# Kernel tuning notes

Measured on AMD Instinct MI355X. Metric: run time of the kernel, lower is better.

Reference implementation:

```python
import jax, jax.numpy as jnp
import numpy as np

B, T, D, H = 2, 2048, 1024, 16
DH = D // H
PD = 6
SCALE = DH ** -0.5
_PAIRS4 = [(0, 1), (0, 2), (0, 3), (1, 2), (1, 3), (2, 3)]
_J6 = jnp.array([[0, 0, 0, 0, 0, 1], [0, 0, 0, 0, -1, 0], [0, 0, 0, 1, 0, 0],
                 [0, 0, 1, 0, 0, 0], [0, -1, 0, 0, 0, 0], [1, 0, 0, 0, 0, 0]], dtype=jnp.float32)


def exterior(p1, p2):
    # p1, p2: (..., 4) -> normalized 6-d Plucker line (..., 6)
    parts = [p1[..., i] * p2[..., j] - p1[..., j] * p2[..., i] for i, j in _PAIRS4]
    L = jnp.stack(parts, axis=-1)
    n = jnp.linalg.norm(L, axis=-1, keepdims=True)
    return L / jnp.clip(n, 1e-12)


def setup_inputs() -> dict:
    key = jax.random.key(0)
    ks = jax.random.split(key, 12)
    s = 0.02
    return {
        'x': jax.random.normal(ks[0], (B, T, D), jnp.float32),
        'qkv_w': jax.random.normal(ks[1], (D, 3 * D), jnp.float32) * s,
        'qkv_b': jnp.zeros((3 * D,), jnp.float32),
        'w1_write': jax.random.normal(ks[2], (D, 4 * H), jnp.float32) * s,
        'w2_write': jax.random.normal(ks[3], (D, 4 * H), jnp.float32) * s,
        'w1_read': jax.random.normal(ks[4], (D, 4 * H), jnp.float32) * s,
        'w2_read': jax.random.normal(ks[5], (D, 4 * H), jnp.float32) * s,
        'memv_w': jax.random.normal(ks[6], (D, D), jnp.float32) * s,
        'memv_b': jnp.zeros((D,), jnp.float32),
        'memg_w': jax.random.normal(ks[7], (D, H), jnp.float32) * s,
        'memg_b': jnp.zeros((H,), jnp.float32),
        'mem_scale': jnp.full((H,), 0.1, jnp.float32),
        'rw_mix': jnp.zeros((), jnp.float32),
        'out_w': jax.random.normal(ks[8], (D, D), jnp.float32) * s,
        'out_b': jnp.zeros((D,), jnp.float32),
        'decay_logits': jnp.full((H,), 4.6, jnp.float32),
    }


def reference(x, qkv_w, qkv_b, w1_write, w2_write, w1_read, w2_read,
              memv_w, memv_b, memg_w, memg_b, mem_scale, rw_mix,
              out_w, out_b, decay_logits):
    # ---- standard causal softmax attention ----
    qkv = (x @ qkv_w + qkv_b).reshape(B, T, 3, H, DH).transpose(2, 0, 3, 1, 4)
    q, k, v = qkv[0], qkv[1], qkv[2]                      # each (B,H,T,DH)
    scores = jnp.einsum('bhtd,bhsd->bhts', q, k) * SCALE
    mask = jnp.triu(jnp.ones((T, T), bool), 1)
    scores = jnp.where(mask[None, None], -jnp.inf, scores)
    attn = jax.nn.softmax(scores, axis=-1)                # dropout=0 (eval)
    seq_out = jnp.einsum('bhts,bhsd->bthd', attn, v).reshape(B, T, D)

    # ---- Plucker lines for write (prev->cur) and read ----
    x_prev = jnp.concatenate([jnp.zeros((B, 1, D), x.dtype), x[:, :-1]], axis=1)
    w1 = (x_prev @ w1_write).reshape(B, T, H, 4)
    w2 = (x @ w2_write).reshape(B, T, H, 4)
    write_lines = exterior(w1, w2)                        # (B,T,H,6)
    r1 = (x @ w1_read).reshape(B, T, H, 4)
    r2 = (x @ w2_read).reshape(B, T, H, 4)
    read_lines = exterior(r1, r2)

    Jw = jnp.einsum('bthi,ij->bhtj', write_lines, _J6)    # (B,H,T,6)
    Jr = jnp.einsum('bthi,ij->bhtj', read_lines, _J6)
    rd = read_lines.transpose(0, 2, 1, 3)                 # (B,H,T,6)

    # ---- decay-weighted cumsum of 6x6 outer-product states ----
    decays = jax.nn.sigmoid(decay_logits)                 # (H,)
    pos = jnp.arange(T, dtype=x.dtype)
    decay_inv = (1.0 / jnp.clip(decays, 1e-6))[:, None] ** pos[None]   # (H,T)
    decay_fwd = decays[:, None] ** pos[None]                           # (H,T)

    def shifted_state(Jv):
        outer = Jv[..., :, None] * Jv[..., None, :]       # (B,H,T,6,6)
        ow = outer * decay_inv[None, :, :, None, None]
        M = jnp.cumsum(ow, axis=2)
        M = jnp.concatenate([jnp.zeros((B, H, 1, PD, PD), x.dtype), M[:, :, :-1]], axis=2)
        return M * decay_fwd[None, :, :, None, None]

    Mw = shifted_state(Jw)
    Mr = shifted_state(Jr)

    score_w = jnp.einsum('bhti,bhtij,bhtj->bht', rd, Mw, rd)
    score_r = jnp.einsum('bhti,bhtij,bhtj->bht', Jw, Mr, Jw)
    alpha = jax.nn.sigmoid(rw_mix)
    mem_score = (1 - alpha) * score_w + alpha * score_r   # (B,H,T)

    mem_val = x @ memv_w + memv_b                         # (B,T,D)
    gate = jax.nn.sigmoid(x @ memg_w + memg_b)            # (B,T,H)
    mem_score_t = mem_score.transpose(0, 2, 1)            # (B,T,H)
    gated = jax.nn.sigmoid(mem_score_t * mem_scale[None, None, :]) * gate
    gated = gated.mean(axis=-1, keepdims=True)            # (B,T,1)

    return (seq_out + gated * mem_val) @ out_w + out_b
```

## Files before the change

### kernel.cpp

```cpp
#include <hip/hip_runtime.h>

#define Bb 2
#define Tt 2048
#define Dd 1024
#define Hh 16
#define LDC 4480

typedef __attribute__((ext_vector_type(8))) short s16x8;
typedef __attribute__((ext_vector_type(4))) float f32x4;
typedef __attribute__((ext_vector_type(8))) _Float16 f16x8;

__device__ __forceinline__ float bf2f(unsigned short u) {
  unsigned v = ((unsigned)u) << 16;
  union { unsigned u; float f; } c; c.u = v; return c.f;
}
__device__ __forceinline__ unsigned short f2bf(float f) {
  union { float f; unsigned u; } c; c.f = f;
  unsigned u = c.u + 0x7fffu + ((c.u >> 16) & 1u);
  return (unsigned short)(u >> 16);
}
__device__ __forceinline__ float sigm(float x) { return 1.f / (1.f + expf(-x)); }

typedef const __attribute__((address_space(1))) void* gas_ptr;
typedef __attribute__((address_space(3))) void* las_ptr;
__device__ __forceinline__ void gload_lds16(const unsigned short* g, unsigned short* l) {
  __builtin_amdgcn_global_load_lds((gas_ptr)g, (las_ptr)l, 16, 0, 0);
}



__global__ __launch_bounds__(256) void prep_kernel(const float* __restrict__ x,
                                                   const float* __restrict__ qkv_w,
                                                   const float* __restrict__ w1w,
                                                   const float* __restrict__ w2w,
                                                   const float* __restrict__ w1r,
                                                   const float* __restrict__ w2r,
                                                   const float* __restrict__ memg_w,
                                                   const float* __restrict__ memv_w,
                                                   const float* __restrict__ out_w,
                                                   const float* __restrict__ qkv_b,
                                                   const float* __restrict__ memg_b,
                                                   const float* __restrict__ memv_b,
                                                   unsigned short* __restrict__ xb,
                                                   unsigned short* __restrict__ WT,
                                                   unsigned short* __restrict__ outT,
                                                   float* __restrict__ biasC) {
  __shared__ float tile[32][33];
  int id = blockIdx.x;
  if (id < 2048) {
    int i = id * 256 + threadIdx.x;
    int row = i >> 7;
    int k8 = i & 127;
    const float4* xv = reinterpret_cast<const float4*>(x + (size_t)i * 8);
    float4 a = xv[0], b = xv[1];
    s16x8 out;
    out[0] = (short)f2bf(a.x); out[1] = (short)f2bf(a.y);
    out[2] = (short)f2bf(a.z); out[3] = (short)f2bf(a.w);
    out[4] = (short)f2bf(b.x); out[5] = (short)f2bf(b.y);
    out[6] = (short)f2bf(b.z); out[7] = (short)f2bf(b.w);
    int mt = row >> 4, kt = k8 >> 2, quad = k8 & 3;
    int lane = (row & 15) + quad * 16;
    *(s16x8*)&xb[(((size_t)mt * 32 + kt) * 64 + lane) * 8] = out;
  } else if (id < 6528) {
    int j = id - 2048;
    int n0 = (j % 140) * 32, kt = j / 140, k0 = kt * 32;
    int tx = threadIdx.x & 31, ty = threadIdx.x >> 5;
#pragma unroll
    for (int i = 0; i < 4; i++) {
      int k = k0 + ty + i * 8, n = n0 + tx;
      float v;
      if (n < 3072)       v = qkv_w[(size_t)k * 3072 + n];
      else if (n < 3136)  v = w1w[k * 64 + (n - 3072)];
      else if (n < 3200)  v = w2w[k * 64 + (n - 3136)];
      else if (n < 3264)  v = w1r[k * 64 + (n - 3200)];
      else if (n < 3328)  v = w2r[k * 64 + (n - 3264)];
      else if (n < 3344)  v = memg_w[k * 16 + (n - 3328)];
      else if (n < 3392)  v = 0.f;
      else if (n < 4416)  v = memv_w[(size_t)k * 1024 + (n - 3392)];
      else                v = 0.f;
      tile[ty + i * 8][tx] = v;
    }
    __syncthreads();
    if (threadIdx.x < 128) {
      int nl = threadIdx.x & 31, quad = threadIdx.x >> 5;
      s16x8 out;
#pragma unroll
      for (int e = 0; e < 8; e++) out[e] = (short)f2bf(tile[quad * 8 + e][nl]);
      int nt = (n0 >> 4) + (nl >> 4);
      int lane = (nl & 15) + quad * 16;
      *(s16x8*)&WT[(((size_t)nt * 32 + kt) * 64 + lane) * 8] = out;
    }
  } else if (id < 7552) {
    int j = id - 6528;
    int n0 = (j & 31) * 32, kt = j >> 5, k0 = kt * 32;
    int tx = threadIdx.x & 31, ty = threadIdx.x >> 5;
#pragma unroll
    for (int i = 0; i < 4; i++) {
      int k = k0 + ty + i * 8, n = n0 + tx;
      tile[ty + i * 8][tx] = out_w[(size_t)k * 1024 + n];
    }
    __syncthreads();
    if (threadIdx.x < 128) {
      int nl = threadIdx.x & 31, quad = threadIdx.x >> 5;
      s16x8 out;
#pragma unroll
      for (int e = 0; e < 8; e++) out[e] = (short)f2bf(tile[quad * 8 + e][nl]);
      int nt = (n0 >> 4) + (nl >> 4);
      int lane = (nl & 15) + quad * 16;
      *(s16x8*)&outT[(((size_t)nt * 32 + kt) * 64 + lane) * 8] = out;
    }
  } else {
    int i = (id - 7552) * 256 + threadIdx.x;
    if (i < LDC) {
      float v = 0.f;
      if (i < 3072) v = qkv_b[i];
      else if (i >= 3328 && i < 3344) v = memg_b[i - 3328];
      else if (i >= 3392 && i < 4416) v = memv_b[i - 3392];
      biasC[i] = v;
    }
  }
}


template <int MODE>
__global__ __launch_bounds__(256) void gemm_frag_kernel(const unsigned short* __restrict__ Af,
                                                        const unsigned short* __restrict__ Bf,
                                                        void* __restrict__ Cout,
                                                        const float* __restrict__ bias) {
  __shared__ __align__(16) unsigned short lds[2][16][512];
  int mTile, nTile;
  if (MODE == 0) {
    const int xx = blockIdx.x & 7, local = blockIdx.x >> 3;
    mTile = (xx >> 1) * 8 + (local & 7);
    nTile = (xx & 1) * 18 + (local >> 3);
    if (nTile >= 35) return;
  } else {
    mTile = blockIdx.x >> 3;
    nTile = blockIdx.x & 7;
  }
  const int lane = threadIdx.x & 63, wid = threadIdx.x >> 6;
  const int quad = lane >> 4, c16 = lane & 15;
  const int wm = wid >> 1, wn = wid & 1;
  const int mt0 = mTile * 8 + wm * 4;
  const int nt0 = nTile * 8 + wn * 4;

  const unsigned short* src[4];
#pragma unroll
  for (int i = 0; i < 4; i++) {
    int f = wid * 4 + i;
    src[i] = ((f < 8) ? (Af + (size_t)(mTile * 8 + f) * 16384)
                      : (Bf + (size_t)(nTile * 8 + (f - 8)) * 16384))
             + (size_t)lane * 8;
  }

  f32x4 acc[4][4] = {};

#pragma unroll
  for (int i = 0; i < 4; i++) gload_lds16(src[i], &lds[0][wid * 4 + i][0]);
  __syncthreads();

  int buf = 0;
  for (int kt = 0; kt < 32; kt++) {
    if (kt + 1 < 32) {
#pragma unroll
      for (int i = 0; i < 4; i++)
        gload_lds16(src[i] + (size_t)(kt + 1) * 512, &lds[buf ^ 1][wid * 4 + i][0]);
    }
    s16x8 a[4], b[4];
#pragma unroll
    for (int i = 0; i < 4; i++) {
      a[i] = *(const s16x8*)&lds[buf][wm * 4 + i][lane * 8];
      b[i] = *(const s16x8*)&lds[buf][8 + wn * 4 + i][lane * 8];
    }
#pragma unroll
    for (int mt = 0; mt < 4; mt++)
#pragma unroll
      for (int nt = 0; nt < 4; nt++)
        acc[mt][nt] = __builtin_amdgcn_mfma_f32_16x16x32_bf16(a[mt], b[nt],
                                                              acc[mt][nt], 0, 0, 0);
    __syncthreads();
    buf ^= 1;
  }

#pragma unroll
  for (int mt = 0; mt < 4; mt++)
#pragma unroll
    for (int nt = 0; nt < 4; nt++) {
      int col = (nt0 + nt) * 16 + c16;
      float bv = bias[col];
#pragma unroll
      for (int r = 0; r < 4; r++) {
        int row = (mt0 + mt) * 16 + quad * 4 + r;
        if (MODE == 0)
          ((unsigned short*)Cout)[(size_t)row * 4480 + col] = f2bf(acc[mt][nt][r] + bv);
        else
          ((float*)Cout)[(size_t)row * 1024 + col] = acc[mt][nt][r] + bv;
      }
    }
}


__device__ __forceinline__ void ext6(const float* p, const float* q, float* L) {
  L[0] = p[0] * q[1] - p[1] * q[0];
  L[1] = p[0] * q[2] - p[2] * q[0];
  L[2] = p[0] * q[3] - p[3] * q[0];
  L[3] = p[1] * q[2] - p[2] * q[1];
  L[4] = p[1] * q[3] - p[3] * q[1];
  L[5] = p[2] * q[3] - p[3] * q[2];
  float n = sqrtf(L[0]*L[0] + L[1]*L[1] + L[2]*L[2] + L[3]*L[3] + L[4]*L[4] + L[5]*L[5]);
  float inv = 1.f / fmaxf(n, 1e-12f);
#pragma unroll
  for (int k = 0; k < 6; k++) L[k] *= inv;
}


__global__ __launch_bounds__(256) void post1_kernel(const unsigned short* __restrict__ Cq,
                                                    unsigned short* __restrict__ Kt,
                                                    unsigned short* __restrict__ Vt,
                                                    float* __restrict__ Jw,
                                                    float* __restrict__ Jr,
                                                    float* __restrict__ rd) {
  __shared__ unsigned short vt[32 * 66];
  int id = blockIdx.x;
  int tid = threadIdx.x;
  if (id < 2048) {
    int kb = id & 63, bh = id >> 6;
    int b = bh >> 4, h = bh & 15;
    size_t tbase = ((size_t)bh * 64 + kb) * 2048;
    {
      int key = tid >> 3, p = tid & 7, dg = p ^ (key & 7);
      size_t src = (size_t)(b * Tt + kb * 32 + key) * LDC + 1024 + h * 64 + dg * 8;
      s16x8 kv = *(const s16x8*)&Cq[src];
      s16x8 kvs;
#pragma unroll
      for (int e = 0; e < 8; e++)
        kvs[e] = (short)f2bf(bf2f((unsigned short)kv[e]) * 0.125f);
      *(s16x8*)&Kt[tbase + (size_t)tid * 8] = kvs;
    }
    {
      int row = tid >> 3, c = tid & 7;
      size_t src = (size_t)(b * Tt + kb * 32 + row) * LDC + 2048 + h * 64 + c * 8;
      s16x8 vv = *(const s16x8*)&Cq[src];
#pragma unroll
      for (int e = 0; e < 8; e++) {
        union { _Float16 hf; unsigned short s; } cv;
        cv.hf = (_Float16)bf2f((unsigned short)vv[e]);
        vt[row * 66 + c * 8 + e] = cv.s;
      }
    }
    __syncthreads();
    {
      int d = tid >> 2, p = tid & 3, cq = p ^ ((d >> 2) & 3);
      s16x8 out;
#pragma unroll
      for (int e = 0; e < 8; e++) {
        int key = ((e >> 2) & 1) * 16 + cq * 4 + (e & 3);
        out[e] = (short)vt[key * 66 + d];
      }
      *(s16x8*)&Vt[tbase + (size_t)tid * 8] = out;
    }
  } else {
    int idx = (id - 2048) * 256 + tid;
    int h = idx & 15, t = (idx >> 4) & 2047, b = idx >> 15;
    size_t row = (size_t)(b * Tt + t) * LDC;
    float w1[4], w2[4], r1[4], r2[4];
#pragma unroll
    for (int k = 0; k < 4; k++) {
      w1[k] = (t > 0) ? bf2f(Cq[row - LDC + 3072 + h * 4 + k]) : 0.f;
      w2[k] = bf2f(Cq[row + 3136 + h * 4 + k]);
      r1[k] = bf2f(Cq[row + 3200 + h * 4 + k]);
      r2[k] = bf2f(Cq[row + 3264 + h * 4 + k]);
    }
    float Lw[6], Lr[6];
    ext6(w1, w2, Lw);
    ext6(r1, r2, Lr);
    size_t ob = ((size_t)(b * Hh + h) * Tt + t) * 6;
    Jw[ob + 0] = Lw[5]; Jw[ob + 1] = -Lw[4]; Jw[ob + 2] = Lw[3];
    Jw[ob + 3] = Lw[2]; Jw[ob + 4] = -Lw[1]; Jw[ob + 5] = Lw[0];
    Jr[ob + 0] = Lr[5]; Jr[ob + 1] = -Lr[4]; Jr[ob + 2] = Lr[3];
    Jr[ob + 3] = Lr[2]; Jr[ob + 4] = -Lr[1]; Jr[ob + 5] = Lr[0];
#pragma unroll
    for (int k = 0; k < 6; k++) rd[ob + k] = Lr[k];
  }
}


__device__ __forceinline__ void do_tile(int ks, int q0, int quad, int c16,
                                        const s16x8& qf0, const s16x8& qf1,
                                        const s16x8 kf[2][2], const f16x8 vb[4],
                                        float& l_i, f32x4 o[4]) {
  f32x4 st0 = {}, st1 = {};
  __builtin_amdgcn_s_setprio(1);
  st0 = __builtin_amdgcn_mfma_f32_16x16x32_bf16(kf[0][0], qf0, st0, 0, 0, 0);
  st0 = __builtin_amdgcn_mfma_f32_16x16x32_bf16(kf[0][1], qf1, st0, 0, 0, 0);
  st1 = __builtin_amdgcn_mfma_f32_16x16x32_bf16(kf[1][0], qf0, st1, 0, 0, 0);
  st1 = __builtin_amdgcn_mfma_f32_16x16x32_bf16(kf[1][1], qf1, st1, 0, 0, 0);
  __builtin_amdgcn_s_setprio(0);
  bool need_mask = (ks + 31 > q0);
  f16x8 pa;
  float lp = 0.f;
#pragma unroll
  for (int r = 0; r < 4; r++) {
    float v0 = st0[r];
    float v1 = st1[r];
    if (need_mask) {
      v0 = (ks + quad * 4 + r      <= q0 + c16) ? v0 : -1e30f;
      v1 = (ks + 16 + quad * 4 + r <= q0 + c16) ? v1 : -1e30f;
    }
    float p0 = __expf(v0);
    float p1 = __expf(v1);
    lp += p0 + p1;
    pa[r]     = (_Float16)p0;
    pa[4 + r] = (_Float16)p1;
  }
  l_i += lp;
  __builtin_amdgcn_s_setprio(1);
#pragma unroll
  for (int nt = 0; nt < 4; nt++)
    o[nt] = __builtin_amdgcn_mfma_f32_16x16x32_f16(pa, vb[nt], o[nt], 0, 0, 0);
  __builtin_amdgcn_s_setprio(0);
}

__global__ __launch_bounds__(128, 2) void attn_kernel(const unsigned short* __restrict__ Cq,
                                                      const unsigned short* __restrict__ Kt,
                                                      const unsigned short* __restrict__ Vt,
                                                      unsigned short* __restrict__ po) {
  __shared__ float mrg[64][69];
  const int id = blockIdx.x;
  const int xcd = id & 7, rest = id >> 3;
  const int j = rest & 31;
  const int bh = ((rest >> 5) << 3) | xcd;
  const int b = bh >> 4, h = bh & 15;
  const int kw = threadIdx.x >> 6, lane = threadIdx.x & 63;
  const int quad = lane >> 4, c16 = lane & 15;
  const int qA0r = j * 32,        qA1r = j * 32 + 16;
  const int qB0r = 2016 - j * 32, qB1r = 2032 - j * 32;
  const int Ttot = 64 - j;
  const int ht = (j >= 16) ? 16 : (32 - j);
  const int t0 = kw ? ht : 0;
  const int t1 = kw ? Ttot : ht;
  const char* Kbase = (const char*)(Kt + (size_t)bh * 64 * 2048);
  const char* Vbase = (const char*)(Vt + (size_t)bh * 64 * 2048);
  const int vK0 = c16 * 128 + ((quad       ^ (c16 & 7)) * 16);
  const int vK1 = c16 * 128 + (((4 + quad) ^ (c16 & 7)) * 16);
  const int vV  = c16 * 64  + ((quad ^ ((c16 >> 2) & 3)) * 16);

  size_t rowA0 = (size_t)(b * Tt + qA0r + c16) * LDC + h * 64;
  size_t rowA1 = (size_t)(b * Tt + qA1r + c16) * LDC + h * 64;
  size_t rowB0 = (size_t)(b * Tt + qB0r + c16) * LDC + h * 64;
  size_t rowB1 = (size_t)(b * Tt + qB1r + c16) * LDC + h * 64;
  s16x8 qa00 = *(const s16x8*)&Cq[rowA0 + quad * 8];
  s16x8 qa01 = *(const s16x8*)&Cq[rowA0 + 32 + quad * 8];
  s16x8 qa10 = *(const s16x8*)&Cq[rowA1 + quad * 8];
  s16x8 qa11 = *(const s16x8*)&Cq[rowA1 + 32 + quad * 8];
  s16x8 qb00 = *(const s16x8*)&Cq[rowB0 + quad * 8];
  s16x8 qb01 = *(const s16x8*)&Cq[rowB0 + 32 + quad * 8];
  s16x8 qb10 = *(const s16x8*)&Cq[rowB1 + quad * 8];
  s16x8 qb11 = *(const s16x8*)&Cq[rowB1 + 32 + quad * 8];

  float lA0 = 0.f, lA1 = 0.f, lB0 = 0.f, lB1 = 0.f;
  f32x4 oA0[4] = {}, oA1[4] = {}, oB0[4] = {}, oB1[4] = {};

  s16x8 kfX[2][2], kfY[2][2];
  f16x8 vbX[4], vbY[4];

#define LOADT(dstK, dstV, kb) do {                                   \
    const char* Kb_ = Kbase + (size_t)(kb) * 4096;                   \
    const char* Vb_ = Vbase + (size_t)(kb) * 4096;                   \
    dstK[0][0] = *(const s16x8*)(Kb_ + vK0);                         \
    dstK[0][1] = *(const s16x8*)(Kb_ + vK1);                         \
    dstK[1][0] = *(const s16x8*)(Kb_ + 2048 + vK0);                  \
    dstK[1][1] = *(const s16x8*)(Kb_ + 2048 + vK1);                  \
    dstV[0] = *(const f16x8*)(Vb_ + vV);                             \
    dstV[1] = *(const f16x8*)(Vb_ + 1024 + vV);                      \
    dstV[2] = *(const f16x8*)(Vb_ + 2048 + vV);                      \
    dstV[3] = *(const f16x8*)(Vb_ + 3072 + vV);                      \
  } while (0)

#define DOTILES(KF, VF, t) do {                                      \
    int ks_ = (t) * 32;                                              \
    do_tile(ks_, qB0r, quad, c16, qb00, qb01, KF, VF, lB0, oB0);     \
    do_tile(ks_, qB1r, quad, c16, qb10, qb11, KF, VF, lB1, oB1);     \
    if ((t) <= j) {                                                  \
      do_tile(ks_, qA0r, quad, c16, qa00, qa01, KF, VF, lA0, oA0);   \
      do_tile(ks_, qA1r, quad, c16, qa10, qa11, KF, VF, lA1, oA1);   \
    }                                                                \
  } while (0)

  LOADT(kfX, vbX, t0);
  for (int t = t0; t < t1; t += 2) {
    if (t + 1 < t1) LOADT(kfY, vbY, t + 1);
    DOTILES(kfX, vbX, t);
    if (t + 1 < t1) {
      if (t + 2 < t1) LOADT(kfX, vbX, t + 2);
      DOTILES(kfY, vbY, t + 1);
    }
  }
#undef DOTILES
#undef LOADT

  if (kw == 1) {
#pragma unroll
    for (int nt = 0; nt < 4; nt++)
#pragma unroll
      for (int r = 0; r < 4; r++) {
        mrg[lane][nt * 4 + r]      = oB0[nt][r];
        mrg[lane][16 + nt * 4 + r] = oB1[nt][r];
        mrg[lane][32 + nt * 4 + r] = oA0[nt][r];
        mrg[lane][48 + nt * 4 + r] = oA1[nt][r];
      }
    mrg[lane][64] = lB0;
    mrg[lane][65] = lB1;
    mrg[lane][66] = lA0;
    mrg[lane][67] = lA1;
  }
  __syncthreads();
  if (kw == 1) return;
#pragma unroll
  for (int nt = 0; nt < 4; nt++)
#pragma unroll
    for (int r = 0; r < 4; r++) {
      oB0[nt][r] += mrg[lane][nt * 4 + r];
      oB1[nt][r] += mrg[lane][16 + nt * 4 + r];
      oA0[nt][r] += mrg[lane][32 + nt * 4 + r];
      oA1[nt][r] += mrg[lane][48 + nt * 4 + r];
    }
  lB0 += mrg[lane][64];
  lB1 += mrg[lane][65];
  lA0 += mrg[lane][66];
  lA1 += mrg[lane][67];

  lB0 += __shfl_xor(lB0, 16, 64); lB0 += __shfl_xor(lB0, 32, 64);
  lB1 += __shfl_xor(lB1, 16, 64); lB1 += __shfl_xor(lB1, 32, 64);
  lA0 += __shfl_xor(lA0, 16, 64); lA0 += __shfl_xor(lA0, 32, 64);
  lA1 += __shfl_xor(lA1, 16, 64); lA1 += __shfl_xor(lA1, 32, 64);
  float invB0 = 1.f / lB0, invB1 = 1.f / lB1;
  float invA0 = 1.f / lA0, invA1 = 1.f / lA1;
#pragma unroll
  for (int r = 0; r < 4; r++) {
    float ivB0 = __shfl(invB0, quad * 4 + r, 64);
    float ivB1 = __shfl(invB1, quad * 4 + r, 64);
    float ivA0 = __shfl(invA0, quad * 4 + r, 64);
    float ivA1 = __shfl(invA1, quad * 4 + r, 64);
    size_t bB0 = (size_t)(b * Tt + qB0r + quad * 4 + r) * Dd + h * 64;
    size_t bB1 = (size_t)(b * Tt + qB1r + quad * 4 + r) * Dd + h * 64;
    size_t bA0 = (size_t)(b * Tt + qA0r + quad * 4 + r) * Dd + h * 64;
    size_t bA1 = (size_t)(b * Tt + qA1r + quad * 4 + r) * Dd + h * 64;
#pragma unroll
    for (int nt = 0; nt < 4; nt++) {
      po[bB0 + nt * 16 + c16] = f2bf(oB0[nt][r] * ivB0);
      po[bB1 + nt * 16 + c16] = f2bf(oB1[nt][r] * ivB1);
      po[bA0 + nt * 16 + c16] = f2bf(oA0[nt][r] * ivA0);
      po[bA1 + nt * 16 + c16] = f2bf(oA1[nt][r] * ivA1);
    }
  }
}


__global__ __launch_bounds__(64) void scanA_kernel(const float* __restrict__ Jw,
                                                   const float* __restrict__ Jr,
                                                   const float* __restrict__ decay_logits,
                                                   float* __restrict__ chunkA) {
  int blk = blockIdx.x;
  int chunk = blk & 15, bh = (blk >> 4) & 31, type = blk >> 9;
  int lane = threadIdx.x;
  const float* V = (type == 0 ? Jw : Jr) + ((size_t)bh * Tt + chunk * 128) * 6;
  __shared__ float v[768];
  for (int i = lane; i < 768; i += 64) v[i] = V[i];
  __syncthreads();
  float d = sigm(decay_logits[bh & 15]);
  int ll = lane < 36 ? lane : 35;
  int i6 = ll / 6, j6 = ll % 6;
  float A = 0.f;
  for (int s = 0; s < 128; s++) A = d * A + v[s * 6 + i6] * v[s * 6 + j6];
  if (lane < 36) chunkA[((size_t)(type * 32 + bh) * 16 + chunk) * 36 + lane] = A;
}


__global__ __launch_bounds__(128) void scanB_kernel(const float* __restrict__ Jw,
                                                    const float* __restrict__ Jr,
                                                    const float* __restrict__ rd,
                                                    const float* __restrict__ chunkA,
                                                    const float* __restrict__ decay_logits,
                                                    float* __restrict__ score_w,
                                                    float* __restrict__ score_r) {
  int blk = blockIdx.x;
  int chunk = blk & 15, bh = (blk >> 4) & 31, type = blk >> 9;
  int tl = threadIdx.x;
  size_t tb = ((size_t)bh * Tt + chunk * 128) * 6;
  const float* U = (type == 0 ? rd : Jw) + tb;
  const float* W = (type == 0 ? Jw : Jr) + tb;
  __shared__ float wv[768];
  __shared__ float Bm[36];
  for (int i = tl; i < 768; i += 128) wv[i] = W[i];
  float d = sigm(decay_logits[bh & 15]);
  if (tl < 36) {
    float dS = powf(d, 128.f);
    float Bv = 0.f;
    size_t base = (size_t)(type * 32 + bh) * 16;
    for (int c = 0; c < chunk; c++)
      Bv = dS * Bv + d * chunkA[(base + c) * 36 + tl];
    Bm[tl] = Bv;
  }
  __syncthreads();
  float u[6];
#pragma unroll
  for (int i = 0; i < 6; i++) u[i] = U[tl * 6 + i];
  float q = 0.f;
#pragma unroll
  for (int i = 0; i < 6; i++) {
    float bi = 0.f;
#pragma unroll
    for (int j = 0; j < 6; j++) bi += Bm[i * 6 + j] * u[j];
    q += u[i] * bi;
  }
  float acc = 0.f;
  for (int s = 0; s < tl; s++) {
    const float* ws = &wv[s * 6];
    float dot = u[0]*ws[0] + u[1]*ws[1] + u[2]*ws[2] + u[3]*ws[3] + u[4]*ws[4] + u[5]*ws[5];
    acc = d * (acc + dot * dot);
  }
  float score = acc + powf(d, (float)tl) * q;
  float* outp = (type == 0 ? score_w : score_r);
  outp[(size_t)bh * Tt + chunk * 128 + tl] = score;
}


__global__ __launch_bounds__(256) void combine_kernel(const unsigned short* __restrict__ po,
                                                      const unsigned short* __restrict__ Cq,
                                                      const float* __restrict__ score_w,
                                                      const float* __restrict__ score_r,
                                                      const float* __restrict__ mem_scale,
                                                      const float* __restrict__ rw_mix,
                                                      unsigned short* __restrict__ fused) {
  __shared__ float tmp[16];
  int rowi = blockIdx.x;
  int b = rowi >> 11, t = rowi & 2047;
  float alpha = sigm(rw_mix[0]);
  if (threadIdx.x < 16) {
    int h = threadIdx.x;
    size_t sh = (size_t)(b * 16 + h) * Tt + t;
    float ms = (1.f - alpha) * score_w[sh] + alpha * score_r[sh];
    float gate = sigm(bf2f(Cq[(size_t)rowi * LDC + 3328 + h]));
    tmp[h] = sigm(ms * mem_scale[h]) * gate;
  }
  __syncthreads();
  float g = 0.f;
#pragma unroll
  for (int h = 0; h < 16; h++) g += tmp[h];
  g *= (1.f / 16.f);
  if (threadIdx.x < 128) {
    int c = threadIdx.x;
    int d0 = c * 8;
    s16x8 ov = *(const s16x8*)&po[((size_t)b * Tt + t) * Dd + d0];
    s16x8 mv = *(const s16x8*)&Cq[(size_t)rowi * LDC + 3392 + d0];
    s16x8 out;
#pragma unroll
    for (int e = 0; e < 8; e++)
      out[e] = (short)f2bf(bf2f((unsigned short)ov[e]) + g * bf2f((unsigned short)mv[e]));
    int mt = rowi >> 4, kt = c >> 2, quad = c & 3;
    int lane = (rowi & 15) + quad * 16;
    *(s16x8*)&fused[(((size_t)mt * 32 + kt) * 64 + lane) * 8] = out;
  }
}


extern "C" void kernel_launch(void* const* d_in, const int* in_sizes, int n_in,
                              void* d_out, int out_size, void* d_ws, size_t ws_size,
                              hipStream_t stream) {
  (void)in_sizes; (void)n_in; (void)out_size; (void)ws_size;
  const float* x         = (const float*)d_in[0];
  const float* qkv_w     = (const float*)d_in[1];
  const float* qkv_b     = (const float*)d_in[2];
  const float* w1w       = (const float*)d_in[3];
  const float* w2w       = (const float*)d_in[4];
  const float* w1r       = (const float*)d_in[5];
  const float* w2r       = (const float*)d_in[6];
  const float* memv_w    = (const float*)d_in[7];
  const float* memv_b    = (const float*)d_in[8];
  const float* memg_w    = (const float*)d_in[9];
  const float* memg_b    = (const float*)d_in[10];
  const float* mem_scale = (const float*)d_in[11];
  const float* rw_mix    = (const float*)d_in[12];
  const float* out_w     = (const float*)d_in[13];
  const float* out_b     = (const float*)d_in[14];
  const float* decay_l   = (const float*)d_in[15];

  char* w = (char*)d_ws;
  unsigned short* xb    = (unsigned short*)(w + 0);
  unsigned short* Kt    = (unsigned short*)(w + 0);
  unsigned short* WT    = (unsigned short*)(w + 8388608);
  unsigned short* Vt    = (unsigned short*)(w + 8388608);
  unsigned short* outT  = (unsigned short*)(w + 17563648);
  float*          biasC = (float*)(w + 19660800);
  unsigned short* Cbuf  = (unsigned short*)(w + 19678720);
  unsigned short* po    = (unsigned short*)(w + 56378880);
  float*          Jw    = (float*)(w + 73680384);
  float*          Jr    = (float*)(w + 75253248);
  float*          rd    = (float*)(w + 76826112);
  float*          chA   = (float*)(w + 78398976);
  float*          sw    = (float*)(w + 78693888);
  float*          sr    = (float*)(w + 78956032);
  unsigned short* fused = (unsigned short*)(w + 79218176);

  prep_kernel<<<7570, 256, 0, stream>>>(x, qkv_w, w1w, w2w, w1r, w2r, memg_w, memv_w,
                                        out_w, qkv_b, memg_b, memv_b,
                                        xb, WT, outT, biasC);

  gemm_frag_kernel<0><<<1152, 256, 0, stream>>>(xb, WT, Cbuf, biasC);

  post1_kernel<<<2304, 256, 0, stream>>>(Cbuf, Kt, Vt, Jw, Jr, rd);
  attn_kernel<<<1024, 128, 0, stream>>>(Cbuf, Kt, Vt, po);
  scanA_kernel<<<1024, 64, 0, stream>>>(Jw, Jr, decay_l, chA);
  scanB_kernel<<<1024, 128, 0, stream>>>(Jw, Jr, rd, chA, decay_l, sw, sr);
  combine_kernel<<<4096, 256, 0, stream>>>(po, Cbuf, sw, sr, mem_scale, rw_mix, fused);

  gemm_frag_kernel<1><<<256, 256, 0, stream>>>(fused, outT, d_out, out_b);
}
```

Measured before the change: 253.5 us.

## Replace input projection GEMM with larger-tile 4-stage pipelined kernel

Swaps the fused QKV/mem projection GEMM for a new kernel with 256x256 output tiles, 512 threads (8 waves), and a 4-deep LDS ring buffer fed by async global-to-LDS loads with vmcnt-gated prefetch three steps ahead. Larger tiles raise operand reuse per LDS load and cut the block count from 1152 to 288, with an XCD-aware tile mapping. The aim is to lower global/LDS traffic and hide load latency in the largest GEMM. The risks are higher register pressure from 32 accumulators per wave, a larger LDS footprint, and fewer blocks than CUs (288 vs 256 CUs yields a partial second wave).

After: 271.7 us. 1.07x slower.

```diff
diff --git a/kernel.cpp b/kernel.cpp
--- a/kernel.cpp
+++ b/kernel.cpp
@@ -122,6 +122,92 @@
 }
 
 
+__global__ __launch_bounds__(512, 2) void gemm_big_kernel(const unsigned short* __restrict__ Af,
+                                                          const unsigned short* __restrict__ Bf,
+                                                          unsigned short* __restrict__ Cout,
+                                                          const float* __restrict__ bias) {
+  __shared__ __align__(16) unsigned short lds[4][32][512];
+  const int blk = blockIdx.x;
+  const int xcd = blk & 7, local = blk >> 3;
+  const int xm = xcd & 3, xn = xcd >> 2;
+  const int mTile = xm * 4 + (local & 3);
+  const int nTile = xn * 9 + (local >> 2);
+  const int lane = threadIdx.x & 63, wid = threadIdx.x >> 6;
+  const int quad = lane >> 4, c16 = lane & 15;
+  const int wm = wid & 3, wn = wid >> 2;
+
+  const unsigned short* src[4];
+#pragma unroll
+  for (int i = 0; i < 4; i++) {
+    int f = wid * 4 + i;
+    src[i] = ((f < 16) ? (Af + (size_t)(mTile * 16 + f) * 16384)
+                       : (Bf + (size_t)(nTile * 16 + (f - 16)) * 16384))
+             + (size_t)lane * 8;
+  }
+
+  f32x4 acc[4][8] = {};
+
+#define STAGE(kt_) {                                                        \
+    const int bb_ = (kt_) & 3;                                              \
+    gload_lds16(src[0] + (size_t)(kt_) * 512, &lds[bb_][wid * 4 + 0][0]);   \
+    gload_lds16(src[1] + (size_t)(kt_) * 512, &lds[bb_][wid * 4 + 1][0]);   \
+    gload_lds16(src[2] + (size_t)(kt_) * 512, &lds[bb_][wid * 4 + 2][0]);   \
+    gload_lds16(src[3] + (size_t)(kt_) * 512, &lds[bb_][wid * 4 + 3][0]);   \
+  }
+
+#define STEP(kt_, VMC) {                                                    \
+    asm volatile("s_waitcnt vmcnt(" #VMC ")" ::: "memory");                 \
+    __builtin_amdgcn_s_barrier();                                           \
+    __builtin_amdgcn_sched_barrier(0);                                      \
+    const int bb_ = (kt_) & 3;                                              \
+    s16x8 a_[4], b_[8];                                                     \
+    _Pragma("unroll") for (int i_ = 0; i_ < 4; i_++)                        \
+      a_[i_] = *(const s16x8*)&lds[bb_][wm * 4 + i_][lane * 8];             \
+    _Pragma("unroll") for (int j_ = 0; j_ < 8; j_++)                        \
+      b_[j_] = *(const s16x8*)&lds[bb_][16 + wn * 8 + j_][lane * 8];        \
+    asm volatile("s_waitcnt lgkmcnt(0)" ::: "memory");                      \
+    __builtin_amdgcn_sched_barrier(0);                                      \
+    __builtin_amdgcn_s_barrier();                                           \
+    __builtin_amdgcn_s_setprio(1);                                          \
+    _Pragma("unroll") for (int i_ = 0; i_ < 4; i_++)                        \
+      _Pragma("unroll") for (int j_ = 0; j_ < 8; j_++)                      \
+        acc[i_][j_] = __builtin_amdgcn_mfma_f32_16x16x32_bf16(a_[i_], b_[j_], \
+                                                              acc[i_][j_], 0, 0, 0); \
+    __builtin_amdgcn_s_setprio(0);                                          \
+  }
+
+  STAGE(0); STAGE(1); STAGE(2);
+  for (int kt = 0; kt < 29; kt++) {
+    STAGE(kt + 3);
+    STEP(kt, 12);
+  }
+  STEP(29, 8);
+  STEP(30, 4);
+  STEP(31, 0);
+
+#undef STEP
+#undef STAGE
+
+#pragma unroll
+  for (int i = 0; i < 4; i++) {
+    int mt = mTile * 16 + wm * 4 + i;
+#pragma unroll
+    for (int j = 0; j < 8; j++) {
+      int nt = nTile * 16 + wn * 8 + j;
+      int col = nt * 16 + c16;
+      if (col < 4480) {
+        float bv = bias[col];
+#pragma unroll
+        for (int r = 0; r < 4; r++) {
+          int row = mt * 16 + quad * 4 + r;
+          Cout[(size_t)row * 4480 + col] = f2bf(acc[i][j][r] + bv);
+        }
+      }
+    }
+  }
+}
+
+
 template <int MODE>
 __global__ __launch_bounds__(256) void gemm_frag_kernel(const unsigned short* __restrict__ Af,
                                                         const unsigned short* __restrict__ Bf,
@@ -607,7 +693,7 @@
                                         out_w, qkv_b, memg_b, memv_b,
                                         xb, WT, outT, biasC);
 
-  gemm_frag_kernel<0><<<1152, 256, 0, stream>>>(xb, WT, Cbuf, biasC);
+  gemm_big_kernel<<<288, 512, 0, stream>>>(xb, WT, Cbuf, biasC);
 
   post1_kernel<<<2304, 256, 0, stream>>>(Cbuf, Kt, Vt, Jw, Jr, rd);
   attn_kernel<<<1024, 128, 0, stream>>>(Cbuf, Kt, Vt, po);
```

## Replace LDS-staged QKV GEMM with register-blocked direct-load fat-tile kernel

Applied to the files above, without the earlier changes.

Adds a new GEMM kernel that loads pre-fragmented A and B tiles straight from global memory into registers with double buffering, skipping LDS. Each wave computes a 4x8 grid of 16x16 MFMA tiles, so each CTA covers a 128x256 output block and the launch drops from 1152 to 576 blocks. The goal is more reuse per load and no LDS staging or barriers. The cost is heavy register use (accumulators plus two fragment buffers), which may cap occupancy or cause spills, and the bf16 output stores are scalar and strided rather than vectorized.

New measurement: 305.4 us. +20.4%, slower.

```diff
diff --git a/kernel.cpp b/kernel.cpp
--- a/kernel.cpp
+++ b/kernel.cpp
@@ -122,6 +122,67 @@
 }
 
 
+__global__ __launch_bounds__(256, 2) void gemm_fat_kernel(const unsigned short* __restrict__ Af,
+                                                          const unsigned short* __restrict__ Bf,
+                                                          unsigned short* __restrict__ Cout,
+                                                          const float* __restrict__ bias) {
+  const int blk = blockIdx.x;
+  const int xcd = blk & 7, local = blk >> 3;
+  const int mTile = (xcd & 3) * 8 + (local & 7);
+  const int nTile = (xcd >> 2) * 9 + (local >> 3);
+  const int lane = threadIdx.x & 63, wid = threadIdx.x >> 6;
+  const int quad = lane >> 4, c16 = lane & 15;
+  const int wm = wid & 1, wn = wid >> 1;
+  const int mt0 = mTile * 8 + wm * 4;
+  const int nt0 = nTile * 16 + wn * 8;
+
+  const unsigned short* Apt = Af + ((size_t)mt0 * 32 * 64 + lane) * 8;
+  const unsigned short* Bpt = Bf + ((size_t)nt0 * 32 * 64 + lane) * 8;
+
+  f32x4 acc[4][8] = {};
+  s16x8 af[2][4];
+  s16x8 bf[2][8];
+#pragma unroll
+  for (int i = 0; i < 4; i++) af[0][i] = *(const s16x8*)(Apt + (size_t)i * 16384);
+#pragma unroll
+  for (int j = 0; j < 8; j++) bf[0][j] = *(const s16x8*)(Bpt + (size_t)j * 16384);
+
+#pragma unroll
+  for (int kt = 0; kt < 32; kt++) {
+    const int cur = kt & 1, nxt = cur ^ 1;
+    if (kt + 1 < 32) {
+      const unsigned short* An = Apt + (size_t)(kt + 1) * 512;
+      const unsigned short* Bn = Bpt + (size_t)(kt + 1) * 512;
+#pragma unroll
+      for (int i = 0; i < 4; i++) af[nxt][i] = *(const s16x8*)(An + (size_t)i * 16384);
+#pragma unroll
+      for (int j = 0; j < 8; j++) bf[nxt][j] = *(const s16x8*)(Bn + (size_t)j * 16384);
+    }
+#pragma unroll
+    for (int i = 0; i < 4; i++)
+#pragma unroll
+      for (int j = 0; j < 8; j++)
+        acc[i][j] = __builtin_amdgcn_mfma_f32_16x16x32_bf16(af[cur][i], bf[cur][j],
+                                                            acc[i][j], 0, 0, 0);
+  }
+
+#pragma unroll
+  for (int i = 0; i < 4; i++)
+#pragma unroll
+    for (int j = 0; j < 8; j++) {
+      if (nt0 + j < 280) {
+        int col = (nt0 + j) * 16 + c16;
+        float bv = bias[col];
+#pragma unroll
+        for (int r = 0; r < 4; r++) {
+          int row = (mt0 + i) * 16 + quad * 4 + r;
+          Cout[(size_t)row * 4480 + col] = f2bf(acc[i][j][r] + bv);
+        }
+      }
+    }
+}
+
+
 template <int MODE>
 __global__ __launch_bounds__(256) void gemm_frag_kernel(const unsigned short* __restrict__ Af,
                                                         const unsigned short* __restrict__ Bf,
@@ -607,7 +668,7 @@
                                         out_w, qkv_b, memg_b, memv_b,
                                         xb, WT, outT, biasC);
 
-  gemm_frag_kernel<0><<<1152, 256, 0, stream>>>(xb, WT, Cbuf, biasC);
+  gemm_fat_kernel<<<576, 256, 0, stream>>>(xb, WT, Cbuf, biasC);
 
   post1_kernel<<<2304, 256, 0, stream>>>(Cbuf, Kt, Vt, Jw, Jr, rd);
   attn_kernel<<<1024, 128, 0, stream>>>(Cbuf, Kt, Vt, po);
```
